# Optimization experiments

Measured on AMD Instinct MI355X. Metric: run time of the kernel, lower is better.

The kernel has to match this reference:

```python
import jax, jax.numpy as jnp
import numpy as np

B, L, DM, DS, DC, E = 2, 1024, 1024, 16, 4, 2
DI = E * DM          # d_inner = 2048
DR = DM // 16        # dt_rank = 64
EPS = 1e-5


def setup_inputs() -> dict:
    key = jax.random.key(0)
    ks = jax.random.split(key, 8)
    s = lambda k, shp, sc: jax.random.normal(k, shp, jnp.float32) * sc
    return {
        "x": s(ks[0], (B, L, DM), 1.0),
        "norm_w": jnp.ones((DM,), jnp.float32),
        "in_proj_w": s(ks[1], (2 * DI, DM), 0.02),
        "conv_w": s(ks[2], (DI, 1, DC), 0.1),        # depthwise kernel [O=DI, I=1, W=DC]
        "conv_b": s(ks[3], (DI,), 0.02),
        "x_proj_w": s(ks[4], (DR + 2 * DS, DI), 0.02),
        "dt_proj_w": s(ks[5], (DI, DR), 0.02),
        "dt_proj_b": s(ks[6], (DI,), 0.02),
        "A_log": jnp.log(jnp.broadcast_to(jnp.arange(1, DS + 1, dtype=jnp.float32), (DI, DS))),
        "D": jnp.ones((DI,), jnp.float32),
        "out_proj_w": s(ks[7], (DM, DI), 0.02),
    }


def reference(x, norm_w, in_proj_w, conv_w, conv_b, x_proj_w,
              dt_proj_w, dt_proj_b, A_log, D, out_proj_w):
    # RMSNorm
    u = x * jax.lax.rsqrt(jnp.mean(x * x, axis=-1, keepdims=True) + EPS) * norm_w

    # in_proj -> [B, L, 2*DI], split into ssm branch and gate
    xz = jnp.einsum('bld,ed->ble', u, in_proj_w)
    xin, z = jnp.split(xz, 2, axis=-1)

    # causal depthwise conv along L + SiLU
    xc = jnp.transpose(xin, (0, 2, 1))                      # [B, DI, L]
    xc = jnp.pad(xc, ((0, 0), (0, 0), (DC - 1, 0)))
    xc = jax.lax.conv_general_dilated(xc, conv_w, (1,), 'VALID',
                                      feature_group_count=DI)  # [B, DI, L]
    xc = jax.nn.silu(xc + conv_b[None, :, None])
    xc = jnp.transpose(xc, (0, 2, 1))                       # [B, L, DI]

    # input-dependent dt, B, C
    dbl = jnp.einsum('bld,ed->ble', xc, x_proj_w)           # [B, L, DR+2*DS]
    dt, Bm, Cm = jnp.split(dbl, [DR, DR + DS], axis=-1)
    delta = jax.nn.softplus(jnp.einsum('blr,dr->bld', dt, dt_proj_w) + dt_proj_b)  # [B,L,DI]

    A = -jnp.exp(A_log)                                     # [DI, DS]
    dA = jnp.exp(delta[..., None] * A)                      # [B, L, DI, DS]
    dBu = delta[..., None] * Bm[:, :, None, :] * xc[..., None]  # [B, L, DI, DS]

    # selective scan: h_t = dA_t * h_{t-1} + dBu_t ; y_t = <h_t, C_t>
    def step(h, inp):
        da, dbu, c = inp
        h = da * h + dbu                                    # [B, DI, DS]
        return h, jnp.einsum('bdn,bn->bd', h, c)

    h0 = jnp.zeros((B, DI, DS), x.dtype)
    _, ys = jax.lax.scan(step, h0,
                         (jnp.swapaxes(dA, 0, 1),
                          jnp.swapaxes(dBu, 0, 1),
                          jnp.swapaxes(Cm, 0, 1)))
    y = jnp.swapaxes(ys, 0, 1) + xc * D                     # [B, L, DI]

    out = jnp.einsum('bld,ed->ble', y * jax.nn.silu(z), out_proj_w)
    return out + x  # residual
```

## Files before the change

kernel.cpp:

```cpp
#include <hip/hip_runtime.h>
#include <math.h>

#define B_   2
#define L_   1024
#define DM   1024
#define DS   16
#define DC   4
#define DI   2048
#define DR   64
#define NTOK (B_*L_)
#define EPSF 1e-5f
#define NC   32
#define CL   (L_/NC)
#define SPLITS 8

typedef __bf16 bf16_t;
typedef bf16_t bf16x4 __attribute__((ext_vector_type(4)));
typedef bf16_t bf16x8 __attribute__((ext_vector_type(8)));
typedef float  f32x4  __attribute__((ext_vector_type(4)));

__device__ __forceinline__ float siluf(float x){ return x / (1.f + __expf(-x)); }
__device__ __forceinline__ float softplusf(float x){ return (x > 20.f) ? x : log1pf(__expf(x)); }

__device__ __forceinline__ void gload_lds16(const void* g, void* l) {
    __builtin_amdgcn_global_load_lds(
        (const __attribute__((address_space(1))) void*)g,
        (__attribute__((address_space(3))) void*)l, 16, 0, 0);
}

struct hl_t { bf16_t h, l; };
__device__ __forceinline__ hl_t split2(float v) {
    hl_t r;
    r.h = (bf16_t)v;
    r.l = (bf16_t)(v - (float)r.h);
    return r;
}

#define SPLIT_IN_BLKS  ((2*DI*DM/4)/256)
#define SPLIT_X_BLKS   ((128*DI/4)/256)
#define SPLIT_O_BLKS   ((DM*DI/4)/256)
__global__ __launch_bounds__(256) void rms_split_all(
    const float* __restrict__ x, const float* __restrict__ w,
    bf16_t* __restrict__ uh, bf16_t* __restrict__ ul,
    const float* __restrict__ in_w, bf16_t* __restrict__ wih, bf16_t* __restrict__ wil,
    const float* __restrict__ x_w,  bf16_t* __restrict__ wxh,  bf16_t* __restrict__ wxl,
    const float* __restrict__ out_w, bf16_t* __restrict__ woh, bf16_t* __restrict__ wol)
{
    __shared__ float sred[4];
    int blk = blockIdx.x;
    int t = threadIdx.x;

    if (blk < NTOK) {
        int row = blk;
        float4 v = ((const float4*)(x + (size_t)row*DM))[t];
        float ss = v.x*v.x + v.y*v.y + v.z*v.z + v.w*v.w;
        #pragma unroll
        for (int off = 32; off > 0; off >>= 1) ss += __shfl_xor(ss, off, 64);
        if ((t & 63) == 0) sred[t >> 6] = ss;
        __syncthreads();
        ss = sred[0] + sred[1] + sred[2] + sred[3];
        float rs = rsqrtf(ss * (1.f/(float)DM) + EPSF);
        float4 wv = ((const float4*)w)[t];
        float o[4];
        o[0] = v.x*rs*wv.x; o[1] = v.y*rs*wv.y; o[2] = v.z*rs*wv.z; o[3] = v.w*rs*wv.w;
        bf16x4 hv, lv;
        #pragma unroll
        for (int j = 0; j < 4; ++j) { hl_t s = split2(o[j]); hv[j] = s.h; lv[j] = s.l; }
        *(bf16x4*)(uh + (size_t)row*DM + t*4) = hv;
        *(bf16x4*)(ul + (size_t)row*DM + t*4) = lv;
        return;
    }
    blk -= NTOK;
    if (blk < SPLIT_IN_BLKS) {
        int i = blk * 256 + t;
        float4 v = ((const float4*)in_w)[i];
        float o[4] = {v.x, v.y, v.z, v.w};
        bf16x4 hv, lv;
        #pragma unroll
        for (int j = 0; j < 4; ++j) { hl_t s = split2(o[j]); hv[j] = s.h; lv[j] = s.l; }
        ((bf16x4*)wih)[i] = hv;
        ((bf16x4*)wil)[i] = lv;
        return;
    }
    blk -= SPLIT_IN_BLKS;
    if (blk < SPLIT_X_BLKS) {
        int i = blk * 256 + t;
        int row = i >> 9;
        bf16x4 hv, lv;
        if (row < 96) {
            float4 v = ((const float4*)x_w)[i];
            float o[4] = {v.x, v.y, v.z, v.w};
            #pragma unroll
            for (int j = 0; j < 4; ++j) { hl_t s = split2(o[j]); hv[j] = s.h; lv[j] = s.l; }
        } else {
            #pragma unroll
            for (int j = 0; j < 4; ++j) { hv[j] = (bf16_t)0.f; lv[j] = (bf16_t)0.f; }
        }
        ((bf16x4*)wxh)[i] = hv;
        ((bf16x4*)wxl)[i] = lv;
        return;
    }
    blk -= SPLIT_X_BLKS;
    {
        int i = blk * 256 + t;
        float4 v = ((const float4*)out_w)[i];
        float o[4] = {v.x, v.y, v.z, v.w};
        bf16x4 hv, lv;
        #pragma unroll
        for (int j = 0; j < 4; ++j) { hl_t s = split2(o[j]); hv[j] = s.h; lv[j] = s.l; }
        ((bf16x4*)woh)[i] = hv;
        ((bf16x4*)wol)[i] = lv;
    }
}

template<int BN, int EPI, bool SK>
__global__ __launch_bounds__(256) void gemm_mfma(
    const bf16_t* __restrict__ Ah, const bf16_t* __restrict__ Al,
    const bf16_t* __restrict__ Bh, const bf16_t* __restrict__ Bl,
    float* __restrict__ C, int ldc,
    const float* __restrict__ res, const float* __restrict__ bias,
    int M, int N, int K, int kspl)
{
    constexpr int NJ   = BN / 32;
    constexpr int WN   = BN / 2;
    constexpr int ACH  = 8;
    constexpr int BCH  = BN / 16;
    constexpr int NCH  = 2*ACH + 2*BCH;
    constexpr int PERW = NCH / 4;
    constexpr int AOFF_L = 128*32;
    constexpr int BOFF_H = 2*128*32;
    constexpr int BOFF_L = 2*128*32 + BN*32;
    constexpr int BUFSZ  = 2*128*32 + 2*BN*32;

    __shared__ bf16_t lds[2*BUFSZ];

    int t = threadIdx.x;
    int w = t >> 6, lane = t & 63;
    int wr = w >> 1, wc = w & 1;
    int m0 = blockIdx.y * 128;
    int n0 = SK ? 0 : blockIdx.x * BN;
    int k0beg = SK ? blockIdx.x * kspl : 0;
    int nst = (SK ? kspl : K) >> 5;
    float* Cp = C;
    if (SK) Cp += (size_t)blockIdx.x * M * BN;

    f32x4 acc[4][NJ];
    #pragma unroll
    for (int i = 0; i < 4; ++i)
        #pragma unroll
        for (int j = 0; j < NJ; ++j)
            acc[i][j] = (f32x4){0.f, 0.f, 0.f, 0.f};

    int lrow = lane >> 2;
    int lcol = (lane & 3) * 8;
    int ar   = wr*64 + (lane & 15);
    int br   = wc*WN + (lane & 15);
    int koff = (lane >> 4) * 8;

    auto STAGE = [&](int buf, int k0) {
        int base = buf ? BUFSZ : 0;
        #pragma unroll
        for (int q = 0; q < PERW; ++q) {
            int ch = w * PERW + q;
            const bf16_t* g; int le;
            if (ch < ACH) {
                int cc = ch;
                g  = Ah + (size_t)(m0 + cc*16 + lrow)*K + k0 + lcol;
                le = cc*512 + lane*8;
            } else if (ch < 2*ACH) {
                int cc = ch - ACH;
                g  = Al + (size_t)(m0 + cc*16 + lrow)*K + k0 + lcol;
                le = AOFF_L + cc*512 + lane*8;
            } else if (ch < 2*ACH + BCH) {
                int cc = ch - 2*ACH;
                g  = Bh + (size_t)(n0 + cc*16 + lrow)*K + k0 + lcol;
                le = BOFF_H + cc*512 + lane*8;
            } else {
                int cc = ch - 2*ACH - BCH;
                g  = Bl + (size_t)(n0 + cc*16 + lrow)*K + k0 + lcol;
                le = BOFF_L + cc*512 + lane*8;
            }
            gload_lds16(g, &lds[base + le]);
        }
    };

    STAGE(0, k0beg);
    __syncthreads();
    int cur = 0;
    for (int s = 0; s < nst; ++s) {
        int k0 = k0beg + (s << 5);
        if (s + 1 < nst) STAGE(cur ^ 1, k0 + 32);
        int base = cur ? BUFSZ : 0;

        bf16x8 ah[4], al4[4], bh[NJ], bl4[NJ];
        #pragma unroll
        for (int i = 0; i < 4; ++i) {
            ah[i]  = *(const bf16x8*)&lds[base + (ar + i*16)*32 + koff];
            al4[i] = *(const bf16x8*)&lds[base + AOFF_L + (ar + i*16)*32 + koff];
        }
        #pragma unroll
        for (int j = 0; j < NJ; ++j) {
            bh[j]  = *(const bf16x8*)&lds[base + BOFF_H + (br + j*16)*32 + koff];
            bl4[j] = *(const bf16x8*)&lds[base + BOFF_L + (br + j*16)*32 + koff];
        }
        #pragma unroll
        for (int i = 0; i < 4; ++i)
            #pragma unroll
            for (int j = 0; j < NJ; ++j) {
                acc[i][j] = __builtin_amdgcn_mfma_f32_16x16x32_bf16(ah[i],  bh[j],  acc[i][j], 0, 0, 0);
                acc[i][j] = __builtin_amdgcn_mfma_f32_16x16x32_bf16(al4[i], bh[j],  acc[i][j], 0, 0, 0);
                acc[i][j] = __builtin_amdgcn_mfma_f32_16x16x32_bf16(ah[i],  bl4[j], acc[i][j], 0, 0, 0);
            }
        __syncthreads();
        cur ^= 1;
    }

    int rb = m0 + wr*64 + (lane >> 4)*4;
    int cb = n0 + wc*WN + (lane & 15);
    #pragma unroll
    for (int i = 0; i < 4; ++i)
        #pragma unroll
        for (int j = 0; j < NJ; ++j) {
            int col = cb + j*16;
            #pragma unroll
            for (int r = 0; r < 4; ++r) {
                int row = rb + i*16 + r;
                float v = acc[i][j][r];
                if (EPI == 2) v += res[(size_t)row*ldc + col];
                Cp[(size_t)row*ldc + col] = v;
            }
        }
}

__global__ __launch_bounds__(256) void dt_fuse(
    const float* __restrict__ parts,
    float* __restrict__ bc,
    const float* __restrict__ dt_w,
    const float* __restrict__ dt_b,
    float* __restrict__ delta)
{
    __shared__ float dtsh[4][DR];
    int blk = blockIdx.x;
    int t = threadIdx.x;
    if (t < 128) {
        int token = t >> 5;
        int c = (t & 31) * 4;
        int m = blk*4 + token;
        float4 s = {0.f, 0.f, 0.f, 0.f};
        #pragma unroll
        for (int sp = 0; sp < SPLITS; ++sp) {
            float4 v = *(const float4*)(parts + ((size_t)sp*NTOK + m)*128 + c);
            s.x += v.x; s.y += v.y; s.z += v.z; s.w += v.w;
        }
        if (c < 64) {
            *(float4*)&dtsh[token][c] = s;
        } else if (c < 96) {
            *(float4*)(bc + (size_t)m*32 + (c - 64)) = s;
        }
    }
    __syncthreads();
    for (int dd = 0; dd < 8; ++dd) {
        int d = dd*256 + t;
        float4 wv[16];
        #pragma unroll
        for (int k4 = 0; k4 < 16; ++k4)
            wv[k4] = *(const float4*)(dt_w + (size_t)d*DR + k4*4);
        float bb = dt_b[d];
        float acc[4];
        #pragma unroll
        for (int tok = 0; tok < 4; ++tok) acc[tok] = bb;
        #pragma unroll
        for (int k4 = 0; k4 < 16; ++k4) {
            #pragma unroll
            for (int tok = 0; tok < 4; ++tok) {
                acc[tok] = fmaf(wv[k4].x, dtsh[tok][k4*4+0], acc[tok]);
                acc[tok] = fmaf(wv[k4].y, dtsh[tok][k4*4+1], acc[tok]);
                acc[tok] = fmaf(wv[k4].z, dtsh[tok][k4*4+2], acc[tok]);
                acc[tok] = fmaf(wv[k4].w, dtsh[tok][k4*4+3], acc[tok]);
            }
        }
        #pragma unroll
        for (int tok = 0; tok < 4; ++tok)
            delta[(size_t)(blk*4 + tok)*DI + d] = softplusf(acc[tok]);
    }
}

__global__ __launch_bounds__(256) void conv_silu_k(const float* __restrict__ xz,
                                                   const float* __restrict__ cw,
                                                   const float* __restrict__ cb,
                                                   bf16_t* __restrict__ xch,
                                                   bf16_t* __restrict__ xcl)
{
    int idx = blockIdx.x * 256 + threadIdx.x;
    int d4 = idx & (DI/4 - 1);
    int m  = idx >> 9;
    int l  = m & (L_ - 1);
    int d  = d4 * 4;

    float4 w0 = *(const float4*)(cw + (size_t)(d+0)*DC);
    float4 w1 = *(const float4*)(cw + (size_t)(d+1)*DC);
    float4 w2 = *(const float4*)(cw + (size_t)(d+2)*DC);
    float4 w3 = *(const float4*)(cw + (size_t)(d+3)*DC);
    float wr0[4] = {w0.x,w0.y,w0.z,w0.w};
    float wr1[4] = {w1.x,w1.y,w1.z,w1.w};
    float wr2[4] = {w2.x,w2.y,w2.z,w2.w};
    float wr3[4] = {w3.x,w3.y,w3.z,w3.w};
    float4 bias = *(const float4*)(cb + d);
    float a0 = bias.x, a1 = bias.y, a2 = bias.z, a3 = bias.w;

    #pragma unroll
    for (int j = 0; j < DC; ++j) {
        int tt = l - (DC-1) + j;
        if (tt < 0) continue;
        float4 xv = *(const float4*)(xz + (size_t)(m - l + tt)*(2*DI) + d);
        a0 = fmaf(wr0[j], xv.x, a0);
        a1 = fmaf(wr1[j], xv.y, a1);
        a2 = fmaf(wr2[j], xv.z, a2);
        a3 = fmaf(wr3[j], xv.w, a3);
    }
    float o[4] = { siluf(a0), siluf(a1), siluf(a2), siluf(a3) };
    bf16x4 hv, lv;
    #pragma unroll
    for (int j = 0; j < 4; ++j) { hl_t s = split2(o[j]); hv[j] = s.h; lv[j] = s.l; }
    *(bf16x4*)(xch + (size_t)m*DI + d) = hv;
    *(bf16x4*)(xcl + (size_t)m*DI + d) = lv;
}

__global__ __launch_bounds__(256) void scan_p1(const float* __restrict__ delta,
                                               const bf16_t* __restrict__ xch,
                                               const bf16_t* __restrict__ xcl,
                                               const float* __restrict__ bc,
                                               const float* __restrict__ A_log,
                                               float* __restrict__ Sbuf,
                                               float* __restrict__ Hbuf)
{
    __shared__ float Bsh[CL][16];
    int t = threadIdx.x;
    int blk = blockIdx.x;
    int d = (blk & 7) * 256 + t;
    int c = (blk >> 3) & (NC - 1);
    int b = blk >> 8;
    int m0 = b * L_ + c * CL;

    for (int i = t; i < CL*16; i += 256)
        Bsh[i >> 4][i & 15] = bc[(size_t)(m0 + (i >> 4))*32 + (i & 15)];
    __syncthreads();

    float A[16], h[16];
    #pragma unroll
    for (int j = 0; j < 4; ++j) {
        float4 al = *(const float4*)(A_log + (size_t)d*DS + j*4);
        A[j*4+0] = -__expf(al.x); A[j*4+1] = -__expf(al.y);
        A[j*4+2] = -__expf(al.z); A[j*4+3] = -__expf(al.w);
    }
    #pragma unroll
    for (int n = 0; n < 16; ++n) h[n] = 0.f;
    float S = 0.f;

    #pragma unroll 4
    for (int tt = 0; tt < CL; ++tt) {
        int m = m0 + tt;
        float dv = delta[(size_t)m*DI + d];
        float xv = (float)xch[(size_t)m*DI + d] + (float)xcl[(size_t)m*DI + d];
        float dx = dv * xv;
        S += dv;
        #pragma unroll
        for (int n = 0; n < 16; ++n) {
            float dA = __expf(dv * A[n]);
            h[n] = fmaf(dA, h[n], Bsh[tt][n] * dx);
        }
    }

    Sbuf[(size_t)(b*NC + c)*DI + d] = S;
    size_t o = ((size_t)((b*NC + c)*DI) + d) * DS;
    #pragma unroll
    for (int j = 0; j < 4; ++j) {
        float4 hv;
        hv.x = h[j*4+0]; hv.y = h[j*4+1]; hv.z = h[j*4+2]; hv.w = h[j*4+3];
        *(float4*)(Hbuf + o + j*4) = hv;
    }
}

__global__ __launch_bounds__(256) void scan_p2(const float* __restrict__ Sbuf,
                                               float* __restrict__ Hbuf,
                                               const float* __restrict__ A_log)
{
    int idx = blockIdx.x * 256 + threadIdx.x;
    int n = idx & 15;
    int d = (idx >> 4) & (DI - 1);
    int b = idx >> 15;
    float Areg = -__expf(A_log[(size_t)d*DS + n]);
    float h = 0.f;
    #pragma unroll
    for (int c = 0; c < NC; ++c) {
        size_t so = (size_t)(b*NC + c)*DI + d;
        size_t o  = so * DS + n;
        float P  = __expf(Areg * Sbuf[so]);
        float hh = Hbuf[o];
        Hbuf[o] = h;
        h = fmaf(P, h, hh);
    }
}

__global__ __launch_bounds__(256) void scan_p3(const float* __restrict__ delta,
                                               const float* __restrict__ xz,
                                               const bf16_t* __restrict__ xch,
                                               const bf16_t* __restrict__ xcl,
                                               const float* __restrict__ bc,
                                               const float* __restrict__ A_log,
                                               const float* __restrict__ Dp,
                                               const float* __restrict__ h0buf,
                                               bf16_t* __restrict__ gh,
                                               bf16_t* __restrict__ gl)
{
    __shared__ float Bsh[CL][16];
    __shared__ float Csh[CL][16];
    int t = threadIdx.x;
    int blk = blockIdx.x;
    int d = (blk & 7) * 256 + t;
    int c = (blk >> 3) & (NC - 1);
    int b = blk >> 8;
    int m0 = b * L_ + c * CL;

    for (int i = t; i < CL*16; i += 256) {
        int tt = i >> 4, n = i & 15;
        size_t ro = (size_t)(m0 + tt)*32;
        Bsh[tt][n] = bc[ro + n];
        Csh[tt][n] = bc[ro + 16 + n];
    }
    __syncthreads();

    float A[16], h[16];
    #pragma unroll
    for (int j = 0; j < 4; ++j) {
        float4 al = *(const float4*)(A_log + (size_t)d*DS + j*4);
        A[j*4+0] = -__expf(al.x); A[j*4+1] = -__expf(al.y);
        A[j*4+2] = -__expf(al.z); A[j*4+3] = -__expf(al.w);
    }
    size_t o = ((size_t)((b*NC + c)*DI) + d) * DS;
    #pragma unroll
    for (int j = 0; j < 4; ++j) {
        float4 hv = *(const float4*)(h0buf + o + j*4);
        h[j*4+0] = hv.x; h[j*4+1] = hv.y; h[j*4+2] = hv.z; h[j*4+3] = hv.w;
    }
    float Dreg = Dp[d];

    for (int t0 = 0; t0 < CL; t0 += 4) {
        float dv[4], xv[4], zv[4];
        #pragma unroll
        for (int q = 0; q < 4; ++q) {
            int m = m0 + t0 + q;
            dv[q] = delta[(size_t)m*DI + d];
            xv[q] = (float)xch[(size_t)m*DI + d] + (float)xcl[(size_t)m*DI + d];
            zv[q] = xz[(size_t)m*(2*DI) + DI + d];
        }
        #pragma unroll
        for (int q = 0; q < 4; ++q) {
            int tt = t0 + q, m = m0 + tt;
            float dx = dv[q] * xv[q];
            float y = 0.f;
            #pragma unroll
            for (int n = 0; n < 16; ++n) {
                float dA = __expf(dv[q] * A[n]);
                h[n] = fmaf(dA, h[n], Bsh[tt][n] * dx);
                y = fmaf(h[n], Csh[tt][n], y);
            }
            float gv = (y + xv[q]*Dreg) * siluf(zv[q]);
            hl_t s = split2(gv);
            gh[(size_t)m*DI + d] = s.h;
            gl[(size_t)m*DI + d] = s.l;
        }
    }
}

extern "C" void kernel_launch(void* const* d_in, const int* in_sizes, int n_in,
                              void* d_out, int out_size, void* d_ws, size_t ws_size,
                              hipStream_t stream)
{
    const float* x         = (const float*)d_in[0];
    const float* norm_w    = (const float*)d_in[1];
    const float* in_proj_w = (const float*)d_in[2];
    const float* conv_w    = (const float*)d_in[3];
    const float* conv_b    = (const float*)d_in[4];
    const float* x_proj_w  = (const float*)d_in[5];
    const float* dt_proj_w = (const float*)d_in[6];
    const float* dt_proj_b = (const float*)d_in[7];
    const float* A_log     = (const float*)d_in[8];
    const float* Dp        = (const float*)d_in[9];
    const float* out_proj_w= (const float*)d_in[10];
    float* out = (float*)d_out;

    char* p = (char*)d_ws;
    float*  xz    = (float*)p;  p += (size_t)NTOK*2*DI*4;
    bf16_t* xch   = (bf16_t*)p; p += (size_t)NTOK*DI*2;
    bf16_t* xcl   = (bf16_t*)p; p += (size_t)NTOK*DI*2;
    float*  delta = (float*)p;  p += (size_t)NTOK*DI*4;
    float*  bc    = (float*)p;  p += (size_t)NTOK*32*4;
    float*  Hbuf  = (float*)p;  p += (size_t)B_*NC*DI*DS*4;
    char*   Wreg  = p;          p += (size_t)2*DI*DM*2*2;
    bf16_t* woh   = (bf16_t*)p; p += (size_t)DM*DI*2;
    bf16_t* wol   = (bf16_t*)p; p += (size_t)DM*DI*2;
    float*  Sbuf  = (float*)p;  p += (size_t)B_*NC*DI*4;
    bf16_t* wxh   = (bf16_t*)p; p += (size_t)128*DI*2;
    bf16_t* wxl   = (bf16_t*)p; p += (size_t)128*DI*2;

    bf16_t* uh  = (bf16_t*)Hbuf;
    bf16_t* ul  = uh + (size_t)NTOK*DM;
    float*  parts = Hbuf;
    bf16_t* wih = (bf16_t*)Wreg;
    bf16_t* wil = wih + (size_t)2*DI*DM;
    bf16_t* gh  = (bf16_t*)Wreg;
    bf16_t* gl  = gh + (size_t)NTOK*DI;

    rms_split_all<<<NTOK + SPLIT_IN_BLKS + SPLIT_X_BLKS + SPLIT_O_BLKS, 256, 0, stream>>>(
        x, norm_w, uh, ul, in_proj_w, wih, wil, x_proj_w, wxh, wxl,
        out_proj_w, woh, wol);

    gemm_mfma<128,0,false><<<dim3((2*DI)/128, NTOK/128), 256, 0, stream>>>(
        uh, ul, wih, wil, xz, 2*DI, nullptr, nullptr, NTOK, 2*DI, DM, 0);

    conv_silu_k<<<(NTOK*(DI/4))/256, 256, 0, stream>>>(xz, conv_w, conv_b, xch, xcl);

    gemm_mfma<128,0,true><<<dim3(SPLITS, NTOK/128), 256, 0, stream>>>(
        xch, xcl, wxh, wxl, parts, 128, nullptr, nullptr, NTOK, 128, DI, DI/SPLITS);

    dt_fuse<<<NTOK/4, 256, 0, stream>>>(parts, bc, dt_proj_w, dt_proj_b, delta);

    scan_p1<<<B_*NC*(DI/256), 256, 0, stream>>>(delta, xch, xcl, bc, A_log, Sbuf, Hbuf);
    scan_p2<<<(B_*DI*DS)/256, 256, 0, stream>>>(Sbuf, Hbuf, A_log);
    scan_p3<<<B_*NC*(DI/256), 256, 0, stream>>>(delta, xz, xch, xcl, bc, A_log, Dp,
                                                Hbuf, gh, gl);

    gemm_mfma<64,2,false><<<dim3(DM/64, NTOK/128), 256, 0, stream>>>(
        gh, gl, woh, wol, out, DM, x, nullptr, NTOK, DM, DI, 0);
}
```

Baseline: 330.5 us.

## Fold chunk-prefix scan into scan_p3 and remap GEMM blocks per XCD

The separate scan_p2 kernel, which combined per-chunk end states sequentially, is removed. Each scan_p3 thread now rebuilds its chunk's initial state by walking all earlier chunk summaries itself, which saves a launch and a write/read pass over Hbuf but adds redundant O(c) work and exps per chunk. The non-split GEMMs also remap block IDs so that consecutive blocks on the same XCD share row/column tiles for better L2 reuse. The unused bias parameter is dropped.

```diff
diff --git a/kernel.cpp b/kernel.cpp
--- a/kernel.cpp
+++ b/kernel.cpp
@@ -118,7 +118,7 @@
     const bf16_t* __restrict__ Ah, const bf16_t* __restrict__ Al,
     const bf16_t* __restrict__ Bh, const bf16_t* __restrict__ Bl,
     float* __restrict__ C, int ldc,
-    const float* __restrict__ res, const float* __restrict__ bias,
+    const float* __restrict__ res,
     int M, int N, int K, int kspl)
 {
     constexpr int NJ   = BN / 32;
@@ -137,12 +137,22 @@
     int t = threadIdx.x;
     int w = t >> 6, lane = t & 63;
     int wr = w >> 1, wc = w & 1;
-    int m0 = blockIdx.y * 128;
-    int n0 = SK ? 0 : blockIdx.x * BN;
-    int k0beg = SK ? blockIdx.x * kspl : 0;
+
+    int bx, by;
+    if (!SK) {
+        int bid = blockIdx.y * gridDim.x + blockIdx.x;
+        int xcd = bid & 7;
+        int i   = bid >> 3;
+        bx = xcd * (int)(gridDim.x >> 3) + (i >> 4);
+        by = i & 15;
+    } else { bx = blockIdx.x; by = blockIdx.y; }
+
+    int m0 = by * 128;
+    int n0 = SK ? 0 : bx * BN;
+    int k0beg = SK ? bx * kspl : 0;
     int nst = (SK ? kspl : K) >> 5;
     float* Cp = C;
-    if (SK) Cp += (size_t)blockIdx.x * M * BN;
+    if (SK) Cp += (size_t)bx * M * BN;
 
     f32x4 acc[4][NJ];
     #pragma unroll
@@ -381,27 +391,6 @@
     }
 }
 
-__global__ __launch_bounds__(256) void scan_p2(const float* __restrict__ Sbuf,
-                                               float* __restrict__ Hbuf,
-                                               const float* __restrict__ A_log)
-{
-    int idx = blockIdx.x * 256 + threadIdx.x;
-    int n = idx & 15;
-    int d = (idx >> 4) & (DI - 1);
-    int b = idx >> 15;
-    float Areg = -__expf(A_log[(size_t)d*DS + n]);
-    float h = 0.f;
-    #pragma unroll
-    for (int c = 0; c < NC; ++c) {
-        size_t so = (size_t)(b*NC + c)*DI + d;
-        size_t o  = so * DS + n;
-        float P  = __expf(Areg * Sbuf[so]);
-        float hh = Hbuf[o];
-        Hbuf[o] = h;
-        h = fmaf(P, h, hh);
-    }
-}
-
 __global__ __launch_bounds__(256) void scan_p3(const float* __restrict__ delta,
                                                const float* __restrict__ xz,
                                                const bf16_t* __restrict__ xch,
@@ -409,7 +398,8 @@
                                                const float* __restrict__ bc,
                                                const float* __restrict__ A_log,
                                                const float* __restrict__ Dp,
-                                               const float* __restrict__ h0buf,
+                                               const float* __restrict__ Sbuf,
+                                               const float* __restrict__ Hbuf,
                                                bf16_t* __restrict__ gh,
                                                bf16_t* __restrict__ gl)
 {
@@ -437,11 +427,21 @@
         A[j*4+0] = -__expf(al.x); A[j*4+1] = -__expf(al.y);
         A[j*4+2] = -__expf(al.z); A[j*4+3] = -__expf(al.w);
     }
-    size_t o = ((size_t)((b*NC + c)*DI) + d) * DS;
-    #pragma unroll
-    for (int j = 0; j < 4; ++j) {
-        float4 hv = *(const float4*)(h0buf + o + j*4);
-        h[j*4+0] = hv.x; h[j*4+1] = hv.y; h[j*4+2] = hv.z; h[j*4+3] = hv.w;
+    #pragma unroll
+    for (int n = 0; n < 16; ++n) h[n] = 0.f;
+    for (int j = 0; j < c; ++j) {
+        size_t so = (size_t)(b*NC + j)*DI + d;
+        float S = Sbuf[so];
+        size_t o = so * DS;
+        float Hj[16];
+        #pragma unroll
+        for (int q = 0; q < 4; ++q) {
+            float4 hv = *(const float4*)(Hbuf + o + q*4);
+            Hj[q*4+0] = hv.x; Hj[q*4+1] = hv.y; Hj[q*4+2] = hv.z; Hj[q*4+3] = hv.w;
+        }
+        #pragma unroll
+        for (int n = 0; n < 16; ++n)
+            h[n] = fmaf(__expf(A[n]*S), h[n], Hj[n]);
     }
     float Dreg = Dp[d];
 
@@ -517,20 +517,19 @@
         out_proj_w, woh, wol);
 
     gemm_mfma<128,0,false><<<dim3((2*DI)/128, NTOK/128), 256, 0, stream>>>(
-        uh, ul, wih, wil, xz, 2*DI, nullptr, nullptr, NTOK, 2*DI, DM, 0);
+        uh, ul, wih, wil, xz, 2*DI, nullptr, NTOK, 2*DI, DM, 0);
 
     conv_silu_k<<<(NTOK*(DI/4))/256, 256, 0, stream>>>(xz, conv_w, conv_b, xch, xcl);
 
     gemm_mfma<128,0,true><<<dim3(SPLITS, NTOK/128), 256, 0, stream>>>(
-        xch, xcl, wxh, wxl, parts, 128, nullptr, nullptr, NTOK, 128, DI, DI/SPLITS);
+        xch, xcl, wxh, wxl, parts, 128, nullptr, NTOK, 128, DI, DI/SPLITS);
 
     dt_fuse<<<NTOK/4, 256, 0, stream>>>(parts, bc, dt_proj_w, dt_proj_b, delta);
 
     scan_p1<<<B_*NC*(DI/256), 256, 0, stream>>>(delta, xch, xcl, bc, A_log, Sbuf, Hbuf);
-    scan_p2<<<(B_*DI*DS)/256, 256, 0, stream>>>(Sbuf, Hbuf, A_log);
     scan_p3<<<B_*NC*(DI/256), 256, 0, stream>>>(delta, xz, xch, xcl, bc, A_log, Dp,
-                                                Hbuf, gh, gl);
+                                                Sbuf, Hbuf, gh, gl);
 
     gemm_mfma<64,2,false><<<dim3(DM/64, NTOK/128), 256, 0, stream>>>(
-        gh, gl, woh, wol, out, DM, x, nullptr, NTOK, DM, DI, 0);
-}
+        gh, gl, woh, wol, out, DM, x, NTOK, DM, DI, 0);
+}
```

New measurement: 333.6 us. Within noise of the previous version (+0.9%).
